# Optimization experiments

Measured on AMD Instinct MI355X. Metric: run time of the kernel, lower is better.

## Reference

```python
import jax, jax.numpy as jnp
from jax import lax
import numpy as np

GROUPS = 32

def setup_inputs() -> dict:
    key = jax.random.key(0)
    ks = jax.random.split(key, 12)
    B, C, H, O, N = 4, 256, 256, 256, 4096
    s = 0.02  # small init scale to keep logits in a stable range
    x  = jax.random.normal(ks[0], (B, C, N), dtype=jnp.float32)
    Wk = jax.random.normal(ks[1], (H, C), dtype=jnp.float32) * s
    bk = jax.random.normal(ks[2], (H,), dtype=jnp.float32) * s
    Wq = jax.random.normal(ks[3], (H, C), dtype=jnp.float32) * s
    bq = jax.random.normal(ks[4], (H,), dtype=jnp.float32) * s
    W1 = jax.random.normal(ks[5], (H, C), dtype=jnp.float32) * s
    b1 = jax.random.normal(ks[6], (H,), dtype=jnp.float32) * s
    # grouped conv1d kernel: (out_ch, in_ch // groups, kw) in 'OIH' layout
    W2 = jax.random.normal(ks[7], (H, H // GROUPS, 3), dtype=jnp.float32) * s
    b2 = jax.random.normal(ks[8], (H,), dtype=jnp.float32) * s
    W3 = jax.random.normal(ks[9], (O, H), dtype=jnp.float32) * s
    b3 = jax.random.normal(ks[10], (O,), dtype=jnp.float32) * s
    return {"x": x, "Wk": Wk, "bk": bk, "Wq": Wq, "bq": bq,
            "W1": W1, "b1": b1, "W2": W2, "b2": b2, "W3": W3, "b3": b3}


def reference(x, Wk, bk, Wq, bq, W1, b1, W2, b2, W3, b3):
    # k: 1x1 conv then permute(0,2,1) -> [B, N, H]
    k = jnp.einsum('hc,bcn->bnh', Wk, x) + bk
    # q: 1x1 conv -> [B, H, N]
    q = jnp.einsum('hc,bcn->bhn', Wq, x) + bq[None, :, None]
    # sim = softmax(k @ q, dim=-2): softmax over the FIRST N axis (rows)
    sim = jax.nn.softmax(jnp.einsum('bnh,bhm->bnm', k, q), axis=-2)  # [B, N, N]
    # v path: 1x1 conv -> grouped 3-tap conv (pad=1) -> ReLU -> 1x1 conv
    v1 = jnp.einsum('hc,bcn->bhn', W1, x) + b1[None, :, None]
    v2 = lax.conv_general_dilated(
        v1, W2, window_strides=(1,), padding='SAME',
        feature_group_count=GROUPS,
        dimension_numbers=('NCH', 'OIH', 'NCH')) + b2[None, :, None]
    v2 = jax.nn.relu(v2)
    v = jnp.einsum('oh,bhn->bon', W3, v2) + b3[None, :, None]  # [B, O, N]
    # out = v @ sim -> [B, O, N]
    return jnp.einsum('bon,bnm->bom', v, sim)
```

## Files before the change

### kernel.cpp

```cpp
#include <hip/hip_runtime.h>


#define B_ 4
#define C_ 256
#define H_ 256
#define O_ 256
#define N_ 4096
#define NSPLIT 4
#define SPAN (N_ / NSPLIT)
#define ITERS (SPAN / 32)

typedef short short8 __attribute__((ext_vector_type(8)));
typedef float floatx4 __attribute__((ext_vector_type(4)));
typedef float floatx16 __attribute__((ext_vector_type(16)));
typedef unsigned uint2v __attribute__((ext_vector_type(2)));

__device__ __forceinline__ unsigned short f2bf(float f) {
  unsigned u = __float_as_uint(f);
  u = (u + 0x7fffu + ((u >> 16) & 1u)) >> 16;
  return (unsigned short)u;
}
__device__ __forceinline__ float bf2f(unsigned short u) {
  return __uint_as_float(((unsigned)u) << 16);
}
__device__ __forceinline__ floatx4 mfma16(short8 a, short8 b, floatx4 c) {
  return __builtin_amdgcn_mfma_f32_16x16x32_bf16(a, b, c, 0, 0, 0);
}
__device__ __forceinline__ floatx16 mfma32(short8 a, short8 b, floatx16 c) {
  return __builtin_amdgcn_mfma_f32_32x32x16_bf16(a, b, c, 0, 0, 0);
}
__device__ __forceinline__ unsigned pack2bf(float a, float b) {
  return __builtin_amdgcn_perm(__float_as_uint(b) + 0x8000u,
                               __float_as_uint(a) + 0x8000u, 0x07060302u);
}

__global__ __launch_bounds__(256) void prep_transpose_kernel(
    const float* __restrict__ x, unsigned short* __restrict__ xt,
    const float* __restrict__ Wk, const float* __restrict__ Wq,
    const float* __restrict__ W1, const float* __restrict__ W3,
    unsigned short* __restrict__ wk, unsigned short* __restrict__ wq,
    unsigned short* __restrict__ w1, unsigned short* __restrict__ w3) {
  __shared__ unsigned short tile[64][66];
  const int gid = blockIdx.x;
  const int t = threadIdx.x;
  if (gid >= 1024) {
    const int i = (gid - 1024) * 256 + t;
    wk[i] = f2bf(Wk[i]);
    wq[i] = f2bf(Wq[i]);
    w1[i] = f2bf(W1[i]);
    w3[i] = f2bf(W3[i]);
    return;
  }
  const int b  = gid >> 8;
  const int ct = (gid >> 6) & 3;
  const int nt = gid & 63;
  const int c0 = ct * 64, n0 = nt * 64;
  const float* xb = x + ((size_t)b * C_ + c0) * N_ + n0;
#pragma unroll
  for (int rr = 0; rr < 4; ++rr) {
    const int c = (t >> 4) + rr * 16;
    const floatx4 v = *reinterpret_cast<const floatx4*>(
        xb + (size_t)c * N_ + (t & 15) * 4);
#pragma unroll
    for (int i = 0; i < 4; ++i) tile[c][(t & 15) * 4 + i] = f2bf(v[i]);
  }
  __syncthreads();
  unsigned short* xo = xt + ((size_t)b * N_ + n0) * C_ + c0;
#pragma unroll
  for (int rr = 0; rr < 2; ++rr) {
    const int nr = (t >> 3) + rr * 32;
    short8 pk;
#pragma unroll
    for (int i = 0; i < 8; ++i) pk[i] = (short)tile[(t & 7) * 8 + i][nr];
    *reinterpret_cast<short8*>(xo + (size_t)nr * C_ + (t & 7) * 8) = pk;
  }
}

__global__ __launch_bounds__(256) void gemm1_kernel(
    const unsigned short* __restrict__ xt,
    const unsigned short* __restrict__ wk, const unsigned short* __restrict__ wq,
    const unsigned short* __restrict__ w1,
    const float* __restrict__ bk, const float* __restrict__ bq,
    const float* __restrict__ b1,
    unsigned short* __restrict__ ko, unsigned short* __restrict__ qo,
    unsigned short* __restrict__ v1o) {
  const int lane = threadIdx.x & 63;
  const int wid  = blockIdx.x * 4 + (threadIdx.x >> 6);
  const int b  = wid >> 9;
  const int r  = wid & 511;
  const int hh = r >> 8;
  const int nt = r & 255;
  const int n0 = nt * 16;
  const int m  = lane & 15;
  const int q  = lane >> 4;

  const unsigned short* xrow = xt + ((size_t)(b * N_) + n0 + m) * C_;
  const unsigned short* Ws[3] = {wk, wq, w1};

  floatx4 acc[3][8];
  const floatx4 z = {0.f, 0.f, 0.f, 0.f};
#pragma unroll
  for (int o = 0; o < 3; ++o)
#pragma unroll
    for (int tt = 0; tt < 8; ++tt) acc[o][tt] = z;

  for (int cs = 0; cs < 8; ++cs) {
    const int cb = cs * 32 + q * 8;
    short8 af = *reinterpret_cast<const short8*>(xrow + cb);
#pragma unroll
    for (int o = 0; o < 3; ++o) {
#pragma unroll
      for (int tt = 0; tt < 8; ++tt) {
        const int h0 = (hh * 8 + tt) * 16;
        short8 bf = *reinterpret_cast<const short8*>(Ws[o] + (h0 + m) * C_ + cb);
        acc[o][tt] = mfma16(af, bf, acc[o][tt]);
      }
    }
  }

#pragma unroll
  for (int tt = 0; tt < 8; ++tt) {
    const int ks16 = hh * 8 + tt;
    const float bias = bk[ks16 * 16 + m];
#pragma unroll
    for (int r2 = 0; r2 < 4; ++r2) {
      const int n = n0 + q * 4 + r2;
      ko[((size_t)(b * 128 + (n >> 5))) * 8192 + ks16 * 512 + (m >> 3) * 256 +
         (n & 31) * 8 + (m & 7)] = f2bf(acc[0][tt][r2] + bias);
    }
  }
  const float* biases[2] = {bq, b1};
  unsigned short* outs[2] = {qo, v1o};
#pragma unroll
  for (int o = 0; o < 2; ++o) {
#pragma unroll
    for (int tt = 0; tt < 8; ++tt) {
      const int h0 = (hh * 8 + tt) * 16;
      const float bias = biases[o][h0 + m];
#pragma unroll
      for (int r2 = 0; r2 < 4; ++r2) {
        const int n = n0 + q * 4 + r2;
        outs[o][(b * N_ + n) * H_ + h0 + m] = f2bf(acc[o + 1][tt][r2] + bias);
      }
    }
  }
}

__global__ __launch_bounds__(256) void convgemm2_kernel(
    const unsigned short* __restrict__ v1, const float* __restrict__ W2,
    const float* __restrict__ b2, const unsigned short* __restrict__ w3,
    const float* __restrict__ b3, unsigned short* __restrict__ vo) {
  __shared__ unsigned short v2L[32][264];

  const int h   = threadIdx.x;
  const int blk = blockIdx.x;
  const int b   = blk >> 7;
  const int nc  = blk & 127;
  const int n0  = nc * 32;
  const int g8  = h & ~7;

  {
    float w[24];
#pragma unroll
    for (int i = 0; i < 24; ++i) w[i] = W2[h * 24 + i];
    const float bias = b2[h];
    const unsigned short* vb = v1 + (size_t)b * (N_ * H_) + g8;

    float fp[8], fc[8], fn[8];
    if (n0 == 0) {
#pragma unroll
      for (int i = 0; i < 8; ++i) fp[i] = 0.f;
    } else {
      short8 u = *reinterpret_cast<const short8*>(vb + (size_t)(n0 - 1) * H_);
#pragma unroll
      for (int i = 0; i < 8; ++i) fp[i] = bf2f((unsigned short)u[i]);
    }
    {
      short8 u = *reinterpret_cast<const short8*>(vb + (size_t)n0 * H_);
#pragma unroll
      for (int i = 0; i < 8; ++i) fc[i] = bf2f((unsigned short)u[i]);
    }
#pragma unroll 1
    for (int ns = 0; ns < 32; ++ns) {
      const int n = n0 + ns;
      if (n + 1 < N_) {
        short8 u = *reinterpret_cast<const short8*>(vb + (size_t)(n + 1) * H_);
#pragma unroll
        for (int i = 0; i < 8; ++i) fn[i] = bf2f((unsigned short)u[i]);
      } else {
#pragma unroll
        for (int i = 0; i < 8; ++i) fn[i] = 0.f;
      }
      float a = bias;
#pragma unroll
      for (int i = 0; i < 8; ++i)
        a += w[i * 3] * fp[i] + w[i * 3 + 1] * fc[i] + w[i * 3 + 2] * fn[i];
      v2L[ns][h] = f2bf(fmaxf(a, 0.f));
#pragma unroll
      for (int i = 0; i < 8; ++i) { fp[i] = fc[i]; fc[i] = fn[i]; }
    }
  }
  __syncthreads();

  const int ln = threadIdx.x & 63;
  const int wv = threadIdx.x >> 6;
  const int m  = ln & 31;
  const int hl = ln >> 5;

  floatx16 acc2[2];
#pragma unroll
  for (int ot = 0; ot < 2; ++ot)
#pragma unroll
    for (int r = 0; r < 16; ++r) acc2[ot][r] = 0.f;

#pragma unroll
  for (int ks = 0; ks < 16; ++ks) {
    short8 bfr = *reinterpret_cast<const short8*>(&v2L[m][ks * 16 + hl * 8]);
#pragma unroll
    for (int ot = 0; ot < 2; ++ot) {
      const int o0 = wv * 64 + ot * 32;
      short8 afr = *reinterpret_cast<const short8*>(
          w3 + (o0 + m) * H_ + ks * 16 + hl * 8);
      acc2[ot] = mfma32(afr, bfr, acc2[ot]);
    }
  }

  const int kn = (m >> 4) & 1;
  const int nl = m & 15;
  unsigned short* vkn = vo + ((size_t)(b * 128 + nc) * 2 + kn) * 4096;
#pragma unroll
  for (int ot = 0; ot < 2; ++ot)
#pragma unroll
    for (int r = 0; r < 16; ++r) {
      const int o = wv * 64 + ot * 32 + (r & 3) + 8 * (r >> 2) + 4 * hl;
      vkn[(o >> 5) * 512 + (nl >> 3) * 256 + (o & 31) * 8 + (nl & 7)] =
          f2bf(acc2[ot][r] + b3[o]);
    }
}

__global__ __launch_bounds__(256, 2) void attn_kernel(
    const unsigned short* __restrict__ kbf, const unsigned short* __restrict__ qbf,
    const unsigned short* __restrict__ vbf,
    unsigned short* __restrict__ pacc, float* __restrict__ pml) {
  __shared__ __attribute__((aligned(16))) char smem[2][32768];

  const int ln  = threadIdx.x & 63;
  const int wv  = threadIdx.x >> 6;
  const int gid = blockIdx.x;
  const int b   = gid & 3;
  const int s   = (gid >> 2) & 3;
  const int mt128 = gid >> 4;
  const int mt32  = mt128 * 4 + wv;
  const int m0  = mt32 * 32;
  const int m   = ln & 31;
  const int hl  = ln >> 5;
  const int lane_base = ln * 16;

  const unsigned short* qrow = qbf + ((size_t)b * N_ + m0 + m) * H_ + hl * 8;
  short8 qf[16];
#pragma unroll
  for (int ks = 0; ks < 16; ++ks)
    qf[ks] = *reinterpret_cast<const short8*>(qrow + ks * 16);

  floatx16 acc[8];
#pragma unroll
  for (int t = 0; t < 8; ++t)
#pragma unroll
    for (int r = 0; r < 16; ++r) acc[t][r] = 0.f;
  float Lp = 0.f;

  auto stage = [&](int bfi, int nc) {
    const size_t row = (size_t)(b * 128 + s * 32 + nc);
    const char* kg = (const char*)(kbf + row * 8192);
    const char* vg = (const char*)(vbf + row * 8192);
    char* lk = &smem[bfi][0];
    char* lv = &smem[bfi][16384];
#pragma unroll
    for (int j = 0; j < 4; ++j) {
      const int ofs = j * 4096 + wv * 1024 + ln * 16;
      __builtin_amdgcn_global_load_lds(
          (const __attribute__((address_space(1))) void*)(kg + ofs),
          (__attribute__((address_space(3))) void*)(lk + ofs), 16, 0, 0);
      __builtin_amdgcn_global_load_lds(
          (const __attribute__((address_space(1))) void*)(vg + ofs),
          (__attribute__((address_space(3))) void*)(lv + ofs), 16, 0, 0);
    }
  };

  stage(0, 0);
  int bufi = 0;

#pragma unroll 1
  for (int nc = 0; nc < ITERS; ++nc) {
    __syncthreads();
    if (nc + 1 < ITERS) stage(bufi ^ 1, nc + 1);

    const char* sk = &smem[bufi][0];
    const char* sv = &smem[bufi][16384];

    floatx16 sacc;
#pragma unroll
    for (int r = 0; r < 16; ++r) sacc[r] = 0.f;
#pragma unroll
    for (int ks = 0; ks < 16; ++ks) {
      short8 kf = *reinterpret_cast<const short8*>(sk + lane_base + ks * 1024);
      sacc = mfma32(kf, qf[ks], sacc);
    }

    short8 pf0, pf1;
#if __has_builtin(__builtin_amdgcn_permlane32_swap)
    unsigned d[8];
#pragma unroll
    for (int i = 0; i < 8; ++i) {
      const float a = __expf(sacc[2 * i]);
      const float bb = __expf(sacc[2 * i + 1]);
      Lp += a + bb;
      d[i] = pack2bf(a, bb);
    }
#pragma unroll
    for (int g = 0; g < 2; ++g) {
      uint2v r0 = __builtin_amdgcn_permlane32_swap(d[4 * g + 0], d[4 * g + 2],
                                                   false, false);
      uint2v r1 = __builtin_amdgcn_permlane32_swap(d[4 * g + 1], d[4 * g + 3],
                                                   false, false);
      d[4 * g + 0] = r0.x; d[4 * g + 2] = r0.y;
      d[4 * g + 1] = r1.x; d[4 * g + 3] = r1.y;
    }
    union { unsigned u[4]; short8 s8; } c0, c1;
    c0.u[0] = d[0]; c0.u[1] = d[1]; c0.u[2] = d[2]; c0.u[3] = d[3];
    c1.u[0] = d[4]; c1.u[1] = d[5]; c1.u[2] = d[6]; c1.u[3] = d[7];
    pf0 = c0.s8;
    pf1 = c1.s8;
#else
    float pv[16];
#pragma unroll
    for (int r = 0; r < 16; ++r) { pv[r] = __expf(sacc[r]); Lp += pv[r]; }
    unsigned wpk[8];
#pragma unroll
    for (int r4 = 0; r4 < 4; ++r4) {
      wpk[r4]     = pack2bf(pv[r4], pv[r4 + 4]);
      wpk[r4 + 4] = pack2bf(pv[r4 + 8], pv[r4 + 12]);
    }
    const int hlsh = hl * 16;
#pragma unroll
    for (int j = 0; j < 8; ++j) {
      const int srcLane = m + ((j >> 2) << 5);
      const int u0 = __shfl((int)wpk[j & 3],       srcLane);
      const int u1 = __shfl((int)wpk[(j & 3) + 4], srcLane);
      pf0[j] = (short)((unsigned)u0 >> hlsh);
      pf1[j] = (short)((unsigned)u1 >> hlsh);
    }
#endif

#pragma unroll
    for (int ot = 0; ot < 8; ++ot) {
      short8 vf0 = *reinterpret_cast<const short8*>(sv + lane_base + ot * 1024);
      short8 vf1 = *reinterpret_cast<const short8*>(
          sv + lane_base + 8192 + ot * 1024);
      acc[ot] = mfma32(vf0, pf0, acc[ot]);
      acc[ot] = mfma32(vf1, pf1, acc[ot]);
    }
    bufi ^= 1;
  }

  float Lv = Lp + __shfl_xor(Lp, 32);
  const float invL = 1.f / Lv;

  const int pwid = (b * 128 + mt32) * NSPLIT + s;
  unsigned short* pa = pacc + (size_t)pwid * (O_ * 32);
#pragma unroll
  for (int ot = 0; ot < 8; ++ot)
#pragma unroll
    for (int r = 0; r < 16; ++r) {
      const int o = ot * 32 + (r & 3) + 8 * (r >> 2) + 4 * hl;
      pa[o * 32 + m] = f2bf(acc[ot][r] * invL);
    }
  if (hl == 0) pml[pwid * 32 + m] = Lv;
}

__global__ __launch_bounds__(256) void combine_kernel(
    const unsigned short* __restrict__ pacc, const float* __restrict__ pml,
    float* __restrict__ out) {
  const int blk = blockIdx.x;
  const int b   = blk >> 7;
  const int mw  = blk & 127;
  const int o   = threadIdx.x;
  const int base = (b * 128 + mw) * NSPLIT;

  __shared__ float w[NSPLIT][32];
  if (threadIdx.x < 32) {
    const int c = threadIdx.x;
    float L[NSPLIT], sum = 0.f;
#pragma unroll
    for (int sp = 0; sp < NSPLIT; ++sp) {
      L[sp] = pml[(base + sp) * 32 + c];
      sum += L[sp];
    }
    const float inv = 1.f / sum;
#pragma unroll
    for (int sp = 0; sp < NSPLIT; ++sp) w[sp][c] = L[sp] * inv;
  }
  __syncthreads();

  float res[32];
#pragma unroll
  for (int c = 0; c < 32; ++c) res[c] = 0.f;
#pragma unroll
  for (int sp = 0; sp < NSPLIT; ++sp) {
    const unsigned short* pa =
        pacc + (size_t)(base + sp) * (O_ * 32) + o * 32;
#pragma unroll
    for (int c8 = 0; c8 < 4; ++c8) {
      short8 u = *reinterpret_cast<const short8*>(pa + c8 * 8);
#pragma unroll
      for (int i = 0; i < 8; ++i)
        res[c8 * 8 + i] =
            fmaf(w[sp][c8 * 8 + i], bf2f((unsigned short)u[i]), res[c8 * 8 + i]);
    }
  }
  float* ob = out + ((size_t)(b * O_ + o)) * N_ + mw * 32;
#pragma unroll
  for (int c4 = 0; c4 < 8; ++c4) {
    floatx4 v4 = {res[c4 * 4], res[c4 * 4 + 1], res[c4 * 4 + 2], res[c4 * 4 + 3]};
    *reinterpret_cast<floatx4*>(ob + c4 * 4) = v4;
  }
}

extern "C" void kernel_launch(void* const* d_in, const int* in_sizes, int n_in,
                              void* d_out, int out_size, void* d_ws, size_t ws_size,
                              hipStream_t stream) {
  const float* x  = (const float*)d_in[0];
  const float* Wk = (const float*)d_in[1];
  const float* bk = (const float*)d_in[2];
  const float* Wq = (const float*)d_in[3];
  const float* bq = (const float*)d_in[4];
  const float* W1 = (const float*)d_in[5];
  const float* b1 = (const float*)d_in[6];
  const float* W2 = (const float*)d_in[7];
  const float* b2 = (const float*)d_in[8];
  const float* W3 = (const float*)d_in[9];
  const float* b3 = (const float*)d_in[10];
  float* out = (float*)d_out;

  char* ws = (char*)d_ws;
  const size_t SZ = (size_t)B_ * N_ * H_ * sizeof(unsigned short);
  unsigned short* wkbf = (unsigned short*)(ws);
  unsigned short* wqbf = (unsigned short*)(ws + 131072);
  unsigned short* w1bf = (unsigned short*)(ws + 262144);
  unsigned short* w3bf = (unsigned short*)(ws + 393216);
  char* base = ws + 524288;
  unsigned short* kbf  = (unsigned short*)(base);
  unsigned short* qbf  = (unsigned short*)(base + SZ);
  unsigned short* vbf  = (unsigned short*)(base + 2 * SZ);
  unsigned short* xtbf = (unsigned short*)(base + 3 * SZ);
  unsigned short* v1bf = (unsigned short*)(base + 4 * SZ);
  unsigned short* pacc = (unsigned short*)(base + 3 * SZ);
  float*          pml  = (float*)(base + 7 * SZ);

  prep_transpose_kernel<<<1280, 256, 0, stream>>>(
      x, xtbf, Wk, Wq, W1, W3, wkbf, wqbf, w1bf, w3bf);
  gemm1_kernel<<<512, 256, 0, stream>>>(xtbf, wkbf, wqbf, w1bf, bk, bq, b1,
                                        kbf, qbf, v1bf);
  convgemm2_kernel<<<512, 256, 0, stream>>>(v1bf, W2, b2, w3bf, b3, vbf);
  attn_kernel<<<512, 256, 0, stream>>>(kbf, qbf, vbf, pacc, pml);
  combine_kernel<<<512, 256, 0, stream>>>(pacc, pml, out);
}
```

Baseline: 248.2 us.

## Software-pipeline QK and PV stages with separate K/V buffers and setprio

```diff
diff --git a/kernel.cpp b/kernel.cpp
--- a/kernel.cpp
+++ b/kernel.cpp
@@ -242,7 +242,7 @@
     const unsigned short* __restrict__ kbf, const unsigned short* __restrict__ qbf,
     const unsigned short* __restrict__ vbf,
     unsigned short* __restrict__ pacc, float* __restrict__ pml) {
-  __shared__ __attribute__((aligned(16))) char smem[2][32768];
+  __shared__ __attribute__((aligned(16))) char smem[4][16384];
 
   const int ln  = threadIdx.x & 63;
   const int wv  = threadIdx.x >> 6;
@@ -269,46 +269,58 @@
     for (int r = 0; r < 16; ++r) acc[t][r] = 0.f;
   float Lp = 0.f;
 
-  auto stage = [&](int bfi, int nc) {
-    const size_t row = (size_t)(b * 128 + s * 32 + nc);
-    const char* kg = (const char*)(kbf + row * 8192);
-    const char* vg = (const char*)(vbf + row * 8192);
+  const size_t row0 = (size_t)(b * 128 + s * 32);
+
+  auto stageK = [&](int bfi, int nc) {
+    const char* kg = (const char*)(kbf + (row0 + nc) * 8192);
     char* lk = &smem[bfi][0];
-    char* lv = &smem[bfi][16384];
 #pragma unroll
     for (int j = 0; j < 4; ++j) {
       const int ofs = j * 4096 + wv * 1024 + ln * 16;
       __builtin_amdgcn_global_load_lds(
           (const __attribute__((address_space(1))) void*)(kg + ofs),
           (__attribute__((address_space(3))) void*)(lk + ofs), 16, 0, 0);
+    }
+  };
+  auto stageV = [&](int bfi, int nc) {
+    const char* vg = (const char*)(vbf + (row0 + nc) * 8192);
+    char* lv = &smem[2 + bfi][0];
+#pragma unroll
+    for (int j = 0; j < 4; ++j) {
+      const int ofs = j * 4096 + wv * 1024 + ln * 16;
       __builtin_amdgcn_global_load_lds(
           (const __attribute__((address_space(1))) void*)(vg + ofs),
           (__attribute__((address_space(3))) void*)(lv + ofs), 16, 0, 0);
     }
   };
 
-  stage(0, 0);
-  int bufi = 0;
-
-#pragma unroll 1
-  for (int nc = 0; nc < ITERS; ++nc) {
-    __syncthreads();
-    if (nc + 1 < ITERS) stage(bufi ^ 1, nc + 1);
-
-    const char* sk = &smem[bufi][0];
-    const char* sv = &smem[bufi][16384];
-
+  short8 pf0, pf1;
+
+  auto qk = [&](const char* sk) -> floatx16 {
     floatx16 sacc;
 #pragma unroll
     for (int r = 0; r < 16; ++r) sacc[r] = 0.f;
+    __builtin_amdgcn_s_setprio(1);
 #pragma unroll
     for (int ks = 0; ks < 16; ++ks) {
       short8 kf = *reinterpret_cast<const short8*>(sk + lane_base + ks * 1024);
       sacc = mfma32(kf, qf[ks], sacc);
     }
-
-    short8 pf0, pf1;
-#if __has_builtin(__builtin_amdgcn_permlane32_swap)
+    return sacc;
+  };
+  auto pv = [&](const char* sv) {
+    __builtin_amdgcn_s_setprio(1);
+#pragma unroll
+    for (int ot = 0; ot < 8; ++ot) {
+      short8 vf0 = *reinterpret_cast<const short8*>(sv + lane_base + ot * 1024);
+      short8 vf1 = *reinterpret_cast<const short8*>(
+          sv + lane_base + 8192 + ot * 1024);
+      acc[ot] = mfma32(vf0, pf0, acc[ot]);
+      acc[ot] = mfma32(vf1, pf1, acc[ot]);
+    }
+    __builtin_amdgcn_s_setprio(0);
+  };
+  auto softmax = [&](floatx16 sacc) {
     unsigned d[8];
 #pragma unroll
     for (int i = 0; i < 8; ++i) {
@@ -331,37 +343,31 @@
     c1.u[0] = d[4]; c1.u[1] = d[5]; c1.u[2] = d[6]; c1.u[3] = d[7];
     pf0 = c0.s8;
     pf1 = c1.s8;
-#else
-    float pv[16];
-#pragma unroll
-    for (int r = 0; r < 16; ++r) { pv[r] = __expf(sacc[r]); Lp += pv[r]; }
-    unsigned wpk[8];
-#pragma unroll
-    for (int r4 = 0; r4 < 4; ++r4) {
-      wpk[r4]     = pack2bf(pv[r4], pv[r4 + 4]);
-      wpk[r4 + 4] = pack2bf(pv[r4 + 8], pv[r4 + 12]);
-    }
-    const int hlsh = hl * 16;
-#pragma unroll
-    for (int j = 0; j < 8; ++j) {
-      const int srcLane = m + ((j >> 2) << 5);
-      const int u0 = __shfl((int)wpk[j & 3],       srcLane);
-      const int u1 = __shfl((int)wpk[(j & 3) + 4], srcLane);
-      pf0[j] = (short)((unsigned)u0 >> hlsh);
-      pf1[j] = (short)((unsigned)u1 >> hlsh);
-    }
-#endif
-
-#pragma unroll
-    for (int ot = 0; ot < 8; ++ot) {
-      short8 vf0 = *reinterpret_cast<const short8*>(sv + lane_base + ot * 1024);
-      short8 vf1 = *reinterpret_cast<const short8*>(
-          sv + lane_base + 8192 + ot * 1024);
-      acc[ot] = mfma32(vf0, pf0, acc[ot]);
-      acc[ot] = mfma32(vf1, pf1, acc[ot]);
-    }
-    bufi ^= 1;
-  }
+  };
+
+  stageK(0, 0);
+  __syncthreads();
+  stageK(1, 1);
+  stageV(0, 0);
+  {
+    floatx16 sacc = qk(&smem[0][0]);
+    __builtin_amdgcn_s_setprio(0);
+    softmax(sacc);
+  }
+
+#pragma unroll 1
+  for (int nc = 1; nc < ITERS; ++nc) {
+    __syncthreads();
+    if (nc + 1 < ITERS) stageK((nc + 1) & 1, nc + 1);
+    stageV(nc & 1, nc);
+
+    floatx16 sacc = qk(&smem[nc & 1][0]);
+    pv(&smem[2 + ((nc - 1) & 1)][0]);
+    softmax(sacc);
+  }
+
+  __syncthreads();
+  pv(&smem[2 + ((ITERS - 1) & 1)][0]);
 
   float Lv = Lp + __shfl_xor(Lp, 32);
   const float invL = 1.f / Lv;
```

Measured after the change: 246.8 us. About the same (-0.5%).

## Widen attention blocks to 8 waves with triple-buffered LDS prefetch and priority hints

Applied to the files above, without the earlier changes.

```diff
diff --git a/kernel.cpp b/kernel.cpp
--- a/kernel.cpp
+++ b/kernel.cpp
@@ -238,19 +238,20 @@
     }
 }
 
-__global__ __launch_bounds__(256, 2) void attn_kernel(
+__global__ __launch_bounds__(512, 2) void attn_kernel(
     const unsigned short* __restrict__ kbf, const unsigned short* __restrict__ qbf,
     const unsigned short* __restrict__ vbf,
     unsigned short* __restrict__ pacc, float* __restrict__ pml) {
-  __shared__ __attribute__((aligned(16))) char smem[2][32768];
-
-  const int ln  = threadIdx.x & 63;
-  const int wv  = threadIdx.x >> 6;
+  __shared__ __attribute__((aligned(16))) char smem[6][16384];
+
+  const int tid = threadIdx.x;
+  const int ln  = tid & 63;
+  const int wv  = tid >> 6;
   const int gid = blockIdx.x;
   const int b   = gid & 3;
   const int s   = (gid >> 2) & 3;
-  const int mt128 = gid >> 4;
-  const int mt32  = mt128 * 4 + wv;
+  const int mt256 = gid >> 4;
+  const int mt32  = mt256 * 8 + wv;
   const int m0  = mt32 * 32;
   const int m   = ln & 31;
   const int hl  = ln >> 5;
@@ -269,15 +270,16 @@
     for (int r = 0; r < 16; ++r) acc[t][r] = 0.f;
   float Lp = 0.f;
 
-  auto stage = [&](int bfi, int nc) {
-    const size_t row = (size_t)(b * 128 + s * 32 + nc);
-    const char* kg = (const char*)(kbf + row * 8192);
-    const char* vg = (const char*)(vbf + row * 8192);
-    char* lk = &smem[bfi][0];
-    char* lv = &smem[bfi][16384];
-#pragma unroll
-    for (int j = 0; j < 4; ++j) {
-      const int ofs = j * 4096 + wv * 1024 + ln * 16;
+  const size_t row0 = (size_t)(b * 128 + s * 32);
+
+  auto stage = [&](int slot, int nc) {
+    const char* kg = (const char*)(kbf + (row0 + nc) * 8192);
+    const char* vg = (const char*)(vbf + (row0 + nc) * 8192);
+    char* lk = &smem[slot][0];
+    char* lv = &smem[3 + slot][0];
+#pragma unroll
+    for (int j = 0; j < 2; ++j) {
+      const int ofs = j * 8192 + tid * 16;
       __builtin_amdgcn_global_load_lds(
           (const __attribute__((address_space(1))) void*)(kg + ofs),
           (__attribute__((address_space(3))) void*)(lk + ofs), 16, 0, 0);
@@ -288,24 +290,35 @@
   };
 
   stage(0, 0);
-  int bufi = 0;
-
+  stage(1, 1);
+
+  int cur = 0;
 #pragma unroll 1
   for (int nc = 0; nc < ITERS; ++nc) {
-    __syncthreads();
-    if (nc + 1 < ITERS) stage(bufi ^ 1, nc + 1);
-
-    const char* sk = &smem[bufi][0];
-    const char* sv = &smem[bufi][16384];
+    if (nc + 1 < ITERS) {
+      asm volatile("s_waitcnt vmcnt(4)\n\ts_barrier" ::: "memory");
+    } else {
+      asm volatile("s_waitcnt vmcnt(0)\n\ts_barrier" ::: "memory");
+    }
+    __builtin_amdgcn_sched_barrier(0);
+    if (nc + 2 < ITERS) {
+      int ps = cur + 2; if (ps >= 3) ps -= 3;
+      stage(ps, nc + 2);
+    }
+
+    const char* sk = &smem[cur][0];
+    const char* sv = &smem[3 + cur][0];
 
     floatx16 sacc;
 #pragma unroll
     for (int r = 0; r < 16; ++r) sacc[r] = 0.f;
+    __builtin_amdgcn_s_setprio(1);
 #pragma unroll
     for (int ks = 0; ks < 16; ++ks) {
       short8 kf = *reinterpret_cast<const short8*>(sk + lane_base + ks * 1024);
       sacc = mfma32(kf, qf[ks], sacc);
     }
+    __builtin_amdgcn_s_setprio(0);
 
     short8 pf0, pf1;
 #if __has_builtin(__builtin_amdgcn_permlane32_swap)
@@ -352,6 +365,7 @@
     }
 #endif
 
+    __builtin_amdgcn_s_setprio(1);
 #pragma unroll
     for (int ot = 0; ot < 8; ++ot) {
       short8 vf0 = *reinterpret_cast<const short8*>(sv + lane_base + ot * 1024);
@@ -360,7 +374,9 @@
       acc[ot] = mfma32(vf0, pf0, acc[ot]);
       acc[ot] = mfma32(vf1, pf1, acc[ot]);
     }
-    bufi ^= 1;
+    __builtin_amdgcn_s_setprio(0);
+
+    cur = (cur == 2) ? 0 : cur + 1;
   }
 
   float Lv = Lp + __shfl_xor(Lp, 32);
@@ -462,6 +478,6 @@
   gemm1_kernel<<<512, 256, 0, stream>>>(xtbf, wkbf, wqbf, w1bf, bk, bq, b1,
                                         kbf, qbf, v1bf);
   convgemm2_kernel<<<512, 256, 0, stream>>>(v1bf, W2, b2, w3bf, b3, vbf);
-  attn_kernel<<<512, 256, 0, stream>>>(kbf, qbf, vbf, pacc, pml);
+  attn_kernel<<<256, 512, 0, stream>>>(kbf, qbf, vbf, pacc, pml);
   combine_kernel<<<512, 256, 0, stream>>>(pacc, pml, out);
 }
```

New measurement: 248.7 us. About the same (+0.2%).
